# Optimization experiments

Hardware: AMD Instinct MI355X
Metric: run time of the kernel (lower is better)

The kernel has to match this reference:

```python
import jax, jax.numpy as jnp
import numpy as np

D_MODEL = 1024
N_HEADS = 16
HEAD_DIM = D_MODEL // N_HEADS  # 64; note: scores use full d_model dots but sqrt(head_dim) scale
WINDOW = 256
B, S = 4, 4096


def _window_starts(seq_len, ws):
    # replicate the torch loop: half-stride overlapping windows
    stride = ws // 2
    starts = []
    for i in range(0, seq_len, stride):
        end = min(i + ws, seq_len)
        start = max(0, end - ws)
        starts.append(start)
        if end == seq_len:
            break
    return np.asarray(starts, dtype=np.int32)


def setup_inputs() -> dict:
    key = jax.random.key(0)
    ks = jax.random.split(key, 9)
    sc = 0.02
    x = jax.random.normal(ks[0], (B, S, D_MODEL), dtype=jnp.float32)
    Wq = jax.random.normal(ks[1], (D_MODEL, D_MODEL), dtype=jnp.float32) * sc
    bq = jnp.zeros((D_MODEL,), jnp.float32)
    Wk = jax.random.normal(ks[2], (D_MODEL, D_MODEL), dtype=jnp.float32) * sc
    bk = jnp.zeros((D_MODEL,), jnp.float32)
    Wv = jax.random.normal(ks[3], (D_MODEL, D_MODEL), dtype=jnp.float32) * sc
    bv = jnp.zeros((D_MODEL,), jnp.float32)
    Wo = jax.random.normal(ks[4], (D_MODEL, D_MODEL), dtype=jnp.float32) * sc
    bo = jnp.zeros((D_MODEL,), jnp.float32)
    return {"x": x, "Wq": Wq, "bq": bq, "Wk": Wk, "bk": bk,
            "Wv": Wv, "bv": bv, "Wo": Wo, "bo": bo}


def reference(x, Wq, bq, Wk, bk, Wv, bv, Wo, bo):
    Bsz, seq, dm = x.shape
    q = x @ Wq + bq  # [B,S,D] (heads are re-flattened in the windowed path anyway)
    k = x @ Wk + bk
    v = x @ Wv + bv

    starts = _window_starts(seq, WINDOW)            # [W]
    idx = starts[:, None] + np.arange(WINDOW)[None]  # [W, ws] static indices
    idx_j = jnp.asarray(idx)

    qw = q[:, idx_j, :]  # [B, W, ws, D]
    kw = k[:, idx_j, :]
    vw = v[:, idx_j, :]

    scale = 1.0 / np.sqrt(HEAD_DIM).astype(np.float32)
    scores = jnp.einsum('bwid,bwjd->bwij', qw, kw) * scale  # full-d_model dots
    attn = jax.nn.softmax(scores, axis=-1)
    ow = jnp.einsum('bwij,bwjd->bwid', attn, vw)  # [B, W, ws, D]

    flat_idx = idx_j.reshape(-1)  # [W*ws]
    out = jnp.zeros_like(q).at[:, flat_idx, :].add(ow.reshape(Bsz, -1, dm))
    counts = jnp.zeros((seq,), jnp.float32).at[flat_idx].add(1.0)
    out = out / counts[None, :, None]  # overlap-add average

    return out @ Wo + bo
```

## Files before the change

### kernel.cpp

```cpp
#include <hip/hip_runtime.h>
#include <hip/hip_bf16.h>

typedef unsigned short u16;
typedef short bf16x8 __attribute__((ext_vector_type(8)));
typedef float f32x4 __attribute__((ext_vector_type(4)));

#define DM     1024
#define SEQ    4096
#define NBATCH 4
#define NWIN   31
#define NTOK   16384

__device__ __forceinline__ u16 f2b(float f) {
  union { float f; unsigned u; } x; x.f = f;
  unsigned r = (x.u + 0x7fffu + ((x.u >> 16) & 1u)) >> 16;
  return (u16)r;
}
__device__ __forceinline__ float b2f(u16 v) {
  union { unsigned u; float f; } x; x.u = ((unsigned)v) << 16; return x.f;
}
__device__ __forceinline__ void gload_lds16(const u16* g, u16* l) {
  __builtin_amdgcn_global_load_lds(
      (const __attribute__((address_space(1))) void*)g,
      (__attribute__((address_space(3))) void*)l, 16, 0, 0);
}

__global__ __launch_bounds__(256) void k_convert(const float* __restrict__ in,
                                                 u16* __restrict__ out, int n4) {
  int i = blockIdx.x * 256 + threadIdx.x;
  if (i >= n4) return;
  float4 v = ((const float4*)in)[i];
  ushort4 o; o.x = f2b(v.x); o.y = f2b(v.y); o.z = f2b(v.z); o.w = f2b(v.w);
  ((ushort4*)out)[i] = o;
}

__global__ __launch_bounds__(256) void k_transpose4(const float* __restrict__ W0,
                                                    const float* __restrict__ W1,
                                                    const float* __restrict__ W2,
                                                    const float* __restrict__ W3,
                                                    u16* __restrict__ Wt) {
  __shared__ float tile[32][33];
  int z = blockIdx.z;
  const float* W = (z == 0) ? W0 : (z == 1) ? W1 : (z == 2) ? W2 : W3;
  u16* dst = Wt + (size_t)z * DM * DM;
  int n0 = blockIdx.x * 32, k0 = blockIdx.y * 32;
  int tx = threadIdx.x, ty = threadIdx.y;
  #pragma unroll
  for (int i = ty; i < 32; i += 8) tile[i][tx] = W[(size_t)(k0 + i) * DM + n0 + tx];
  __syncthreads();
  #pragma unroll
  for (int i = ty; i < 32; i += 8) dst[(size_t)(n0 + i) * DM + k0 + tx] = f2b(tile[tx][i]);
}

__global__ __launch_bounds__(256) void k_catbias(const float* __restrict__ bq,
                                                 const float* __restrict__ bk,
                                                 const float* __restrict__ bv,
                                                 float* __restrict__ o) {
  int i = blockIdx.x * 256 + threadIdx.x;
  if (i >= 3 * DM) return;
  float v = (i < DM) ? bq[i] : (i < 2 * DM) ? bk[i - DM] : bv[i - 2 * DM];
  o[i] = v;
}

__global__ __launch_bounds__(256, 4) void k_gemm(const u16* __restrict__ A, const u16* __restrict__ Bt,
                                                 const float* __restrict__ bias,
                                                 float* __restrict__ Cf,
                                                 u16* __restrict__ Cb, int ldc,
                                                 u16* __restrict__ Ct, int csplit,
                                                 int M, int N, int K) {
  __shared__ u16 As[128 * 64];
  __shared__ u16 Bs[128 * 64];
  const int tid = threadIdx.x;
  const int wv = tid >> 6, lane = tid & 63;
  const int quad = lane >> 4, l16 = lane & 15;
  const int lr8 = lane >> 3;
  const int lc8 = (((lane & 7) ^ (lr8 & 7)) * 8);
  const int m0 = blockIdx.y * 128, n0 = blockIdx.x * 128;
  const int wm = (wv >> 1) * 64, wn = (wv & 1) * 64;
  const int k7 = l16 & 7;
  f32x4 acc[4][4];
  #pragma unroll
  for (int a = 0; a < 4; ++a)
    #pragma unroll
    for (int b = 0; b < 4; ++b) acc[a][b] = (f32x4){0.f, 0.f, 0.f, 0.f};

  for (int kk = 0; kk < K; kk += 64) {
    #pragma unroll
    for (int j = 0; j < 4; ++j) {
      int e = wv * 4 + j;
      gload_lds16(A + (size_t)(m0 + e * 8 + lr8) * K + kk + lc8, As + e * 512);
    }
    #pragma unroll
    for (int j = 0; j < 4; ++j) {
      int e = wv * 4 + j;
      gload_lds16(Bt + (size_t)(n0 + e * 8 + lr8) * K + kk + lc8, Bs + e * 512);
    }
    __syncthreads();
    #pragma unroll
    for (int h = 0; h < 2; ++h) {
      bf16x8 af[4], bfr[4];
      #pragma unroll
      for (int t = 0; t < 4; ++t)
        af[t]  = *(const bf16x8*)&As[(wm + t * 16 + l16) * 64 + ((h * 4 + quad) ^ k7) * 8];
      #pragma unroll
      for (int t = 0; t < 4; ++t)
        bfr[t] = *(const bf16x8*)&Bs[(wn + t * 16 + l16) * 64 + ((h * 4 + quad) ^ k7) * 8];
      #pragma unroll
      for (int mt = 0; mt < 4; ++mt)
        #pragma unroll
        for (int nt = 0; nt < 4; ++nt)
          acc[mt][nt] = __builtin_amdgcn_mfma_f32_16x16x32_bf16(af[mt], bfr[nt], acc[mt][nt], 0, 0, 0);
    }
    __syncthreads();
  }
  #pragma unroll
  for (int mt = 0; mt < 4; ++mt) {
    #pragma unroll
    for (int nt = 0; nt < 4; ++nt) {
      int row = m0 + wm + mt * 16 + quad * 4;
      int col = n0 + wn + nt * 16 + l16;
      float bv = bias[col];
      if (Cf) {
        #pragma unroll
        for (int r = 0; r < 4; ++r)
          Cf[(size_t)(row + r) * N + col] = acc[mt][nt][r] + bv;
      } else if (col < csplit) {
        #pragma unroll
        for (int r = 0; r < 4; ++r)
          Cb[(size_t)(row + r) * ldc + col] = f2b(acc[mt][nt][r] + bv);
      } else {
        ushort4 o;
        o.x = f2b(acc[mt][nt][0] + bv); o.y = f2b(acc[mt][nt][1] + bv);
        o.z = f2b(acc[mt][nt][2] + bv); o.w = f2b(acc[mt][nt][3] + bv);
        *(ushort4*)&Ct[(size_t)(col - csplit) * M + row] = o;
      }
    }
  }
}

#define LDQ  2048
__global__ __launch_bounds__(256, 2) void k_attn(const u16* __restrict__ QKb, const u16* __restrict__ Vt,
                                                 u16* __restrict__ oA, u16* __restrict__ oB) {
  __shared__ u16 stage[20480];
  __shared__ u16 Pbuf[64 * 256];
  __shared__ float red[2][4][64];
  u16* Qs = stage;
  u16* Ks = stage + 4096;
  u16* Vs = stage;

  const int tid = threadIdx.x;
  const int wv = tid >> 6, lane = tid & 63;
  const int quad = lane >> 4, l16 = lane & 15;
  const int l7 = lane & 7, lr8 = lane >> 3;
  const int kq = (l16 & 7) + (l16 >> 3);

  int id = blockIdx.x;
  int s_ = id >> 3;
  int qt = s_ & 3;
  int pair = (s_ >> 2) * 8 + (id & 7);
  if (pair >= NWIN * NBATCH) return;
  int b = pair / NWIN, w = pair - NWIN * b;

  const int s0 = w * 128;
  const size_t base2 = (size_t)b * SEQ * LDQ;
  const size_t base  = (size_t)b * SEQ * DM;
  const size_t btok  = (size_t)b * SEQ;
  const int qrow0 = s0 + qt * 64;

  f32x4 acc[4][4];
  #pragma unroll
  for (int mt = 0; mt < 4; ++mt)
    #pragma unroll
    for (int nt = 0; nt < 4; ++nt) acc[mt][nt] = (f32x4){0.f, 0.f, 0.f, 0.f};

  for (int kk = 0; kk < DM; kk += 64) {
    #pragma unroll
    for (int j = 0; j < 10; ++j) {
      int idx = wv * 10 + j;
      if (idx < 8) {
        int lc = (l7 ^ ((lr8 + idx) & 7)) * 8;
        gload_lds16(QKb + base2 + (size_t)(qrow0 + idx * 8 + lr8) * LDQ + kk + lc, Qs + idx * 512);
      } else {
        int f = idx - 8;
        int lc = (l7 ^ ((lr8 + f) & 7)) * 8;
        gload_lds16(QKb + DM + base2 + (size_t)(s0 + f * 8 + lr8) * LDQ + kk + lc, Ks + f * 512);
      }
    }
    __syncthreads();
    #pragma unroll
    for (int s2 = 0; s2 < 2; ++s2) {
      bf16x8 aq[4], bk[4];
      #pragma unroll
      for (int mt = 0; mt < 4; ++mt)
        aq[mt] = *(const bf16x8*)&Qs[(mt * 16 + l16) * 64 + (((s2 * 4 + quad) ^ ((kq + 2 * mt) & 7)) * 8)];
      #pragma unroll
      for (int nt = 0; nt < 4; ++nt)
        bk[nt] = *(const bf16x8*)&Ks[(wv * 64 + nt * 16 + l16) * 64 + (((s2 * 4 + quad) ^ ((kq + 2 * nt) & 7)) * 8)];
      #pragma unroll
      for (int mt = 0; mt < 4; ++mt)
        #pragma unroll
        for (int nt = 0; nt < 4; ++nt)
          acc[mt][nt] = __builtin_amdgcn_mfma_f32_16x16x32_bf16(aq[mt], bk[nt], acc[mt][nt], 0, 0, 0);
    }
    __syncthreads();
  }

  float mx[4][4], sm[4][4];
  #pragma unroll
  for (int mt = 0; mt < 4; ++mt)
    #pragma unroll
    for (int r = 0; r < 4; ++r) mx[mt][r] = -1e30f;
  #pragma unroll
  for (int mt = 0; mt < 4; ++mt)
    #pragma unroll
    for (int nt = 0; nt < 4; ++nt)
      #pragma unroll
      for (int r = 0; r < 4; ++r) {
        float v = acc[mt][nt][r] * 0.125f;
        acc[mt][nt][r] = v;
        mx[mt][r] = fmaxf(mx[mt][r], v);
      }
  #pragma unroll
  for (int mt = 0; mt < 4; ++mt)
    #pragma unroll
    for (int r = 0; r < 4; ++r)
      #pragma unroll
      for (int off = 8; off > 0; off >>= 1)
        mx[mt][r] = fmaxf(mx[mt][r], __shfl_xor(mx[mt][r], off, 64));
  if (l16 == 0) {
    #pragma unroll
    for (int mt = 0; mt < 4; ++mt)
      #pragma unroll
      for (int r = 0; r < 4; ++r)
        red[0][wv][mt * 16 + quad * 4 + r] = mx[mt][r];
  }
  __syncthreads();
  float gm[4][4];
  #pragma unroll
  for (int mt = 0; mt < 4; ++mt)
    #pragma unroll
    for (int r = 0; r < 4; ++r) {
      int q = mt * 16 + quad * 4 + r;
      gm[mt][r] = fmaxf(fmaxf(red[0][0][q], red[0][1][q]), fmaxf(red[0][2][q], red[0][3][q]));
      sm[mt][r] = 0.f;
    }
  #pragma unroll
  for (int mt = 0; mt < 4; ++mt)
    #pragma unroll
    for (int nt = 0; nt < 4; ++nt)
      #pragma unroll
      for (int r = 0; r < 4; ++r) {
        float e = __expf(acc[mt][nt][r] - gm[mt][r]);
        acc[mt][nt][r] = e;
        sm[mt][r] += e;
      }
  #pragma unroll
  for (int mt = 0; mt < 4; ++mt)
    #pragma unroll
    for (int r = 0; r < 4; ++r)
      #pragma unroll
      for (int off = 8; off > 0; off >>= 1)
        sm[mt][r] += __shfl_xor(sm[mt][r], off, 64);
  if (l16 == 0) {
    #pragma unroll
    for (int mt = 0; mt < 4; ++mt)
      #pragma unroll
      for (int r = 0; r < 4; ++r)
        red[1][wv][mt * 16 + quad * 4 + r] = sm[mt][r];
  }
  __syncthreads();
  #pragma unroll
  for (int mt = 0; mt < 4; ++mt)
    #pragma unroll
    for (int r = 0; r < 4; ++r) {
      int q = mt * 16 + quad * 4 + r;
      float inv = 1.f / (red[1][0][q] + red[1][1][q] + red[1][2][q] + red[1][3][q]);
      #pragma unroll
      for (int nt = 0; nt < 4; ++nt) {
        int ke = wv * 64 + nt * 16 + l16;
        int phys = (ke >> 3) ^ (q & 7);
        Pbuf[q * 256 + phys * 8 + (ke & 7)] = f2b(acc[mt][nt][r] * inv);
      }
    }
  __syncthreads();

  u16* op = ((w & 1) ? oB : oA) + base;
  for (int slab = 0; slab < 4; ++slab) {
    const int nb = slab * 256;
    f32x4 acc2[4][4];
    #pragma unroll
    for (int mt = 0; mt < 4; ++mt)
      #pragma unroll
      for (int u = 0; u < 4; ++u) acc2[mt][u] = (f32x4){0.f, 0.f, 0.f, 0.f};
    for (int sk = 0; sk < 4; ++sk) {
      const int tok0 = sk * 64;
      #pragma unroll
      for (int j = 0; j < 8; ++j) {
        int e = wv * 8 + j;
        int lc = (l7 ^ ((lr8 + e) & 7)) * 8;
        gload_lds16(Vt + (size_t)(nb + e * 8 + lr8) * NTOK + btok + s0 + tok0 + lc, Vs + e * 512);
      }
      __syncthreads();
      #pragma unroll
      for (int s2 = 0; s2 < 2; ++s2) {
        bf16x8 af[4];
        #pragma unroll
        for (int mt = 0; mt < 4; ++mt) {
          int cP = sk * 8 + s2 * 4 + quad;
          int phys = cP ^ (l16 & 7);
          af[mt] = *(const bf16x8*)&Pbuf[(mt * 16 + l16) * 256 + phys * 8];
        }
        #pragma unroll
        for (int u = 0; u < 4; ++u) {
          bf16x8 bb = *(const bf16x8*)&Vs[(wv * 64 + u * 16 + l16) * 64 +
                                          (((s2 * 4 + quad) ^ ((kq + 2 * u) & 7)) * 8)];
          #pragma unroll
          for (int mt = 0; mt < 4; ++mt)
            acc2[mt][u] = __builtin_amdgcn_mfma_f32_16x16x32_bf16(af[mt], bb, acc2[mt][u], 0, 0, 0);
        }
      }
      __syncthreads();
    }
    #pragma unroll
    for (int mt = 0; mt < 4; ++mt)
      #pragma unroll
      for (int u = 0; u < 4; ++u) {
        int row = qrow0 + mt * 16 + quad * 4;
        int col = nb + wv * 64 + u * 16 + l16;
        #pragma unroll
        for (int r = 0; r < 4; ++r)
          op[(size_t)(row + r) * DM + col] = f2b(acc2[mt][u][r]);
      }
  }
}

__global__ __launch_bounds__(256) void k_norm(const u16* __restrict__ oA, const u16* __restrict__ oB,
                                              u16* __restrict__ out, int n8) {
  int i = blockIdx.x * 256 + threadIdx.x;
  if (i >= n8) return;
  int s = (i >> 7) & (SEQ - 1);
  uint4 a = ((const uint4*)oA)[i];
  uint4 r = a;
  if (s >= 128 && s < 3968) {
    uint4 bq = ((const uint4*)oB)[i];
    const unsigned* ap = (const unsigned*)&a;
    const unsigned* bp = (const unsigned*)&bq;
    unsigned* rp = (unsigned*)&r;
    #pragma unroll
    for (int k = 0; k < 4; ++k) {
      float lo = 0.5f * (b2f((u16)(ap[k] & 0xffff)) + b2f((u16)(bp[k] & 0xffff)));
      float hi = 0.5f * (b2f((u16)(ap[k] >> 16))    + b2f((u16)(bp[k] >> 16)));
      rp[k] = (unsigned)f2b(lo) | ((unsigned)f2b(hi) << 16);
    }
  }
  ((uint4*)out)[i] = r;
}

extern "C" void kernel_launch(void* const* d_in, const int* in_sizes, int n_in,
                              void* d_out, int out_size, void* d_ws, size_t ws_size,
                              hipStream_t stream) {
  const float* x  = (const float*)d_in[0];
  const float* Wq = (const float*)d_in[1];
  const float* bq = (const float*)d_in[2];
  const float* Wk = (const float*)d_in[3];
  const float* bk = (const float*)d_in[4];
  const float* Wv = (const float*)d_in[5];
  const float* bv = (const float*)d_in[6];
  const float* Wo = (const float*)d_in[7];
  const float* bo = (const float*)d_in[8];
  float* out = (float*)d_out;

  char* ws = (char*)d_ws;
  const size_t MB = 1024 * 1024;
  u16*   xb   = (u16*)(ws);
  u16*   qkb  = (u16*)(ws + 32 * MB);
  u16*   vtb  = (u16*)(ws + 96 * MB);
  u16*   wqt  = (u16*)(ws + 128 * MB);
  float* bcat = (float*)(ws + 136 * MB);
  u16*   oA   = (u16*)(ws + 137 * MB);
  u16*   oB   = (u16*)(ws + 169 * MB);

  int n4tok = (int)((size_t)NTOK * DM / 4);
  k_convert<<<(n4tok + 255) / 256, 256, 0, stream>>>(x, xb, n4tok);
  k_transpose4<<<dim3(DM / 32, DM / 32, 4), dim3(32, 8), 0, stream>>>(Wq, Wk, Wv, Wo, wqt);
  k_catbias<<<12, 256, 0, stream>>>(bq, bk, bv, bcat);

  k_gemm<<<dim3(3 * DM / 128, NTOK / 128), 256, 0, stream>>>(
      xb, wqt, bcat, nullptr, qkb, 2048, vtb, 2048, NTOK, 3 * DM, DM);

  k_attn<<<512, 256, 0, stream>>>(qkb, vtb, oA, oB);

  int n8tok = (int)((size_t)NTOK * DM / 8);
  k_norm<<<(n8tok + 255) / 256, 256, 0, stream>>>(oA, oB, xb, n8tok);

  u16* wot = wqt + 3 * (size_t)DM * DM;
  k_gemm<<<dim3(DM / 128, NTOK / 128), 256, 0, stream>>>(
      xb, wot, bo, out, nullptr, DM, nullptr, DM, NTOK, DM, DM);
}
```

Before: 363.4 us.

## Halve attention query tile to 32 rows and fuse prep kernels

The attention kernel now handles 32 query rows per block instead of 64. This doubles the grid to 1024 blocks, shrinks the LDS footprint and register use, and raises the occupancy hint from 2 to 3 blocks. The cost is that the K and V window tiles are loaded twice as often from global memory, so each loaded tile is reused less. Separately, the x conversion, weight transposes and bias concatenation are merged into a single launch to remove launch overhead.

Result: slower. 390.8 us (+7.5%).

```diff
diff --git a/kernel.cpp b/kernel.cpp
--- a/kernel.cpp
+++ b/kernel.cpp
@@ -25,41 +25,42 @@
       (__attribute__((address_space(3))) void*)l, 16, 0, 0);
 }
 
-__global__ __launch_bounds__(256) void k_convert(const float* __restrict__ in,
-                                                 u16* __restrict__ out, int n4) {
-  int i = blockIdx.x * 256 + threadIdx.x;
-  if (i >= n4) return;
-  float4 v = ((const float4*)in)[i];
-  ushort4 o; o.x = f2b(v.x); o.y = f2b(v.y); o.z = f2b(v.z); o.w = f2b(v.w);
-  ((ushort4*)out)[i] = o;
-}
-
-__global__ __launch_bounds__(256) void k_transpose4(const float* __restrict__ W0,
-                                                    const float* __restrict__ W1,
-                                                    const float* __restrict__ W2,
-                                                    const float* __restrict__ W3,
-                                                    u16* __restrict__ Wt) {
+__global__ __launch_bounds__(256) void k_prep(const float* __restrict__ x,
+                                              const float* __restrict__ Wq,
+                                              const float* __restrict__ Wk,
+                                              const float* __restrict__ Wv,
+                                              const float* __restrict__ Wo,
+                                              const float* __restrict__ bq,
+                                              const float* __restrict__ bk,
+                                              const float* __restrict__ bv,
+                                              u16* __restrict__ xb, u16* __restrict__ Wt,
+                                              float* __restrict__ bcat) {
   __shared__ float tile[32][33];
-  int z = blockIdx.z;
-  const float* W = (z == 0) ? W0 : (z == 1) ? W1 : (z == 2) ? W2 : W3;
-  u16* dst = Wt + (size_t)z * DM * DM;
-  int n0 = blockIdx.x * 32, k0 = blockIdx.y * 32;
-  int tx = threadIdx.x, ty = threadIdx.y;
-  #pragma unroll
-  for (int i = ty; i < 32; i += 8) tile[i][tx] = W[(size_t)(k0 + i) * DM + n0 + tx];
-  __syncthreads();
-  #pragma unroll
-  for (int i = ty; i < 32; i += 8) dst[(size_t)(n0 + i) * DM + k0 + tx] = f2b(tile[tx][i]);
-}
-
-__global__ __launch_bounds__(256) void k_catbias(const float* __restrict__ bq,
-                                                 const float* __restrict__ bk,
-                                                 const float* __restrict__ bv,
-                                                 float* __restrict__ o) {
-  int i = blockIdx.x * 256 + threadIdx.x;
-  if (i >= 3 * DM) return;
-  float v = (i < DM) ? bq[i] : (i < 2 * DM) ? bk[i - DM] : bv[i - 2 * DM];
-  o[i] = v;
+  const int id = blockIdx.x, tid = threadIdx.x;
+  if (id < 16384) {
+    int i = id * 256 + tid;
+    float4 v = ((const float4*)x)[i];
+    ushort4 o; o.x = f2b(v.x); o.y = f2b(v.y); o.z = f2b(v.z); o.w = f2b(v.w);
+    ((ushort4*)xb)[i] = o;
+  } else if (id < 20480) {
+    int l = id - 16384;
+    int z = l >> 10, rem = l & 1023;
+    const float* W = (z == 0) ? Wq : (z == 1) ? Wk : (z == 2) ? Wv : Wo;
+    u16* dst = Wt + (size_t)z * DM * DM;
+    int n0 = (rem & 31) * 32, k0 = (rem >> 5) * 32;
+    int tx = tid & 31, ty = tid >> 5;
+    #pragma unroll
+    for (int i = ty; i < 32; i += 8) tile[i][tx] = W[(size_t)(k0 + i) * DM + n0 + tx];
+    __syncthreads();
+    #pragma unroll
+    for (int i = ty; i < 32; i += 8) dst[(size_t)(n0 + i) * DM + k0 + tx] = f2b(tile[tx][i]);
+  } else {
+    int i = (id - 20480) * 256 + tid;
+    if (i < 3 * DM) {
+      float v = (i < DM) ? bq[i] : (i < 2 * DM) ? bk[i - DM] : bv[i - 2 * DM];
+      bcat[i] = v;
+    }
+  }
 }
 
 __global__ __launch_bounds__(256, 4) void k_gemm(const u16* __restrict__ A, const u16* __restrict__ Bt,
@@ -139,13 +140,13 @@
 }
 
 #define LDQ  2048
-__global__ __launch_bounds__(256, 2) void k_attn(const u16* __restrict__ QKb, const u16* __restrict__ Vt,
+__global__ __launch_bounds__(256, 3) void k_attn(const u16* __restrict__ QKb, const u16* __restrict__ Vt,
                                                  u16* __restrict__ oA, u16* __restrict__ oB) {
-  __shared__ u16 stage[20480];
-  __shared__ u16 Pbuf[64 * 256];
-  __shared__ float red[2][4][64];
+  __shared__ u16 stage[18432];
+  __shared__ u16 Pbuf[32 * 256];
+  __shared__ float red[2][4][32];
   u16* Qs = stage;
-  u16* Ks = stage + 4096;
+  u16* Ks = stage + 2048;
   u16* Vs = stage;
 
   const int tid = threadIdx.x;
@@ -156,8 +157,8 @@
 
   int id = blockIdx.x;
   int s_ = id >> 3;
-  int qt = s_ & 3;
-  int pair = (s_ >> 2) * 8 + (id & 7);
+  int qt = s_ & 7;
+  int pair = (s_ >> 3) * 8 + (id & 7);
   if (pair >= NWIN * NBATCH) return;
   int b = pair / NWIN, w = pair - NWIN * b;
 
@@ -165,23 +166,23 @@
   const size_t base2 = (size_t)b * SEQ * LDQ;
   const size_t base  = (size_t)b * SEQ * DM;
   const size_t btok  = (size_t)b * SEQ;
-  const int qrow0 = s0 + qt * 64;
-
-  f32x4 acc[4][4];
-  #pragma unroll
-  for (int mt = 0; mt < 4; ++mt)
+  const int qrow0 = s0 + qt * 32;
+
+  f32x4 acc[2][4];
+  #pragma unroll
+  for (int mt = 0; mt < 2; ++mt)
     #pragma unroll
     for (int nt = 0; nt < 4; ++nt) acc[mt][nt] = (f32x4){0.f, 0.f, 0.f, 0.f};
 
   for (int kk = 0; kk < DM; kk += 64) {
     #pragma unroll
-    for (int j = 0; j < 10; ++j) {
-      int idx = wv * 10 + j;
-      if (idx < 8) {
+    for (int j = 0; j < 9; ++j) {
+      int idx = wv * 9 + j;
+      if (idx < 4) {
         int lc = (l7 ^ ((lr8 + idx) & 7)) * 8;
         gload_lds16(QKb + base2 + (size_t)(qrow0 + idx * 8 + lr8) * LDQ + kk + lc, Qs + idx * 512);
       } else {
-        int f = idx - 8;
+        int f = idx - 4;
         int lc = (l7 ^ ((lr8 + f) & 7)) * 8;
         gload_lds16(QKb + DM + base2 + (size_t)(s0 + f * 8 + lr8) * LDQ + kk + lc, Ks + f * 512);
       }
@@ -189,15 +190,15 @@
     __syncthreads();
     #pragma unroll
     for (int s2 = 0; s2 < 2; ++s2) {
-      bf16x8 aq[4], bk[4];
-      #pragma unroll
-      for (int mt = 0; mt < 4; ++mt)
+      bf16x8 aq[2], bk[4];
+      #pragma unroll
+      for (int mt = 0; mt < 2; ++mt)
         aq[mt] = *(const bf16x8*)&Qs[(mt * 16 + l16) * 64 + (((s2 * 4 + quad) ^ ((kq + 2 * mt) & 7)) * 8)];
       #pragma unroll
       for (int nt = 0; nt < 4; ++nt)
         bk[nt] = *(const bf16x8*)&Ks[(wv * 64 + nt * 16 + l16) * 64 + (((s2 * 4 + quad) ^ ((kq + 2 * nt) & 7)) * 8)];
       #pragma unroll
-      for (int mt = 0; mt < 4; ++mt)
+      for (int mt = 0; mt < 2; ++mt)
         #pragma unroll
         for (int nt = 0; nt < 4; ++nt)
           acc[mt][nt] = __builtin_amdgcn_mfma_f32_16x16x32_bf16(aq[mt], bk[nt], acc[mt][nt], 0, 0, 0);
@@ -205,13 +206,13 @@
     __syncthreads();
   }
 
-  float mx[4][4], sm[4][4];
-  #pragma unroll
-  for (int mt = 0; mt < 4; ++mt)
+  float mx[2][4], sm[2][4];
+  #pragma unroll
+  for (int mt = 0; mt < 2; ++mt)
     #pragma unroll
     for (int r = 0; r < 4; ++r) mx[mt][r] = -1e30f;
   #pragma unroll
-  for (int mt = 0; mt < 4; ++mt)
+  for (int mt = 0; mt < 2; ++mt)
     #pragma unroll
     for (int nt = 0; nt < 4; ++nt)
       #pragma unroll
@@ -221,7 +222,7 @@
         mx[mt][r] = fmaxf(mx[mt][r], v);
       }
   #pragma unroll
-  for (int mt = 0; mt < 4; ++mt)
+  for (int mt = 0; mt < 2; ++mt)
     #pragma unroll
     for (int r = 0; r < 4; ++r)
       #pragma unroll
@@ -229,15 +230,15 @@
         mx[mt][r] = fmaxf(mx[mt][r], __shfl_xor(mx[mt][r], off, 64));
   if (l16 == 0) {
     #pragma unroll
-    for (int mt = 0; mt < 4; ++mt)
+    for (int mt = 0; mt < 2; ++mt)
       #pragma unroll
       for (int r = 0; r < 4; ++r)
         red[0][wv][mt * 16 + quad * 4 + r] = mx[mt][r];
   }
   __syncthreads();
-  float gm[4][4];
-  #pragma unroll
-  for (int mt = 0; mt < 4; ++mt)
+  float gm[2][4];
+  #pragma unroll
+  for (int mt = 0; mt < 2; ++mt)
     #pragma unroll
     for (int r = 0; r < 4; ++r) {
       int q = mt * 16 + quad * 4 + r;
@@ -245,7 +246,7 @@
       sm[mt][r] = 0.f;
     }
   #pragma unroll
-  for (int mt = 0; mt < 4; ++mt)
+  for (int mt = 0; mt < 2; ++mt)
     #pragma unroll
     for (int nt = 0; nt < 4; ++nt)
       #pragma unroll
@@ -255,7 +256,7 @@
         sm[mt][r] += e;
       }
   #pragma unroll
-  for (int mt = 0; mt < 4; ++mt)
+  for (int mt = 0; mt < 2; ++mt)
     #pragma unroll
     for (int r = 0; r < 4; ++r)
       #pragma unroll
@@ -263,14 +264,14 @@
         sm[mt][r] += __shfl_xor(sm[mt][r], off, 64);
   if (l16 == 0) {
     #pragma unroll
-    for (int mt = 0; mt < 4; ++mt)
+    for (int mt = 0; mt < 2; ++mt)
       #pragma unroll
       for (int r = 0; r < 4; ++r)
         red[1][wv][mt * 16 + quad * 4 + r] = sm[mt][r];
   }
   __syncthreads();
   #pragma unroll
-  for (int mt = 0; mt < 4; ++mt)
+  for (int mt = 0; mt < 2; ++mt)
     #pragma unroll
     for (int r = 0; r < 4; ++r) {
       int q = mt * 16 + quad * 4 + r;
@@ -287,9 +288,9 @@
   u16* op = ((w & 1) ? oB : oA) + base;
   for (int slab = 0; slab < 4; ++slab) {
     const int nb = slab * 256;
-    f32x4 acc2[4][4];
-    #pragma unroll
-    for (int mt = 0; mt < 4; ++mt)
+    f32x4 acc2[2][4];
+    #pragma unroll
+    for (int mt = 0; mt < 2; ++mt)
       #pragma unroll
       for (int u = 0; u < 4; ++u) acc2[mt][u] = (f32x4){0.f, 0.f, 0.f, 0.f};
     for (int sk = 0; sk < 4; ++sk) {
@@ -303,9 +304,9 @@
       __syncthreads();
       #pragma unroll
       for (int s2 = 0; s2 < 2; ++s2) {
-        bf16x8 af[4];
-        #pragma unroll
-        for (int mt = 0; mt < 4; ++mt) {
+        bf16x8 af[2];
+        #pragma unroll
+        for (int mt = 0; mt < 2; ++mt) {
           int cP = sk * 8 + s2 * 4 + quad;
           int phys = cP ^ (l16 & 7);
           af[mt] = *(const bf16x8*)&Pbuf[(mt * 16 + l16) * 256 + phys * 8];
@@ -315,14 +316,14 @@
           bf16x8 bb = *(const bf16x8*)&Vs[(wv * 64 + u * 16 + l16) * 64 +
                                           (((s2 * 4 + quad) ^ ((kq + 2 * u) & 7)) * 8)];
           #pragma unroll
-          for (int mt = 0; mt < 4; ++mt)
+          for (int mt = 0; mt < 2; ++mt)
             acc2[mt][u] = __builtin_amdgcn_mfma_f32_16x16x32_bf16(af[mt], bb, acc2[mt][u], 0, 0, 0);
         }
       }
       __syncthreads();
     }
     #pragma unroll
-    for (int mt = 0; mt < 4; ++mt)
+    for (int mt = 0; mt < 2; ++mt)
       #pragma unroll
       for (int u = 0; u < 4; ++u) {
         int row = qrow0 + mt * 16 + quad * 4;
@@ -380,15 +381,12 @@
   u16*   oA   = (u16*)(ws + 137 * MB);
   u16*   oB   = (u16*)(ws + 169 * MB);
 
-  int n4tok = (int)((size_t)NTOK * DM / 4);
-  k_convert<<<(n4tok + 255) / 256, 256, 0, stream>>>(x, xb, n4tok);
-  k_transpose4<<<dim3(DM / 32, DM / 32, 4), dim3(32, 8), 0, stream>>>(Wq, Wk, Wv, Wo, wqt);
-  k_catbias<<<12, 256, 0, stream>>>(bq, bk, bv, bcat);
+  k_prep<<<20492, 256, 0, stream>>>(x, Wq, Wk, Wv, Wo, bq, bk, bv, xb, wqt, bcat);
 
   k_gemm<<<dim3(3 * DM / 128, NTOK / 128), 256, 0, stream>>>(
       xb, wqt, bcat, nullptr, qkb, 2048, vtb, 2048, NTOK, 3 * DM, DM);
 
-  k_attn<<<512, 256, 0, stream>>>(qkb, vtb, oA, oB);
+  k_attn<<<1024, 256, 0, stream>>>(qkb, vtb, oA, oB);
 
   int n8tok = (int)((size_t)NTOK * DM / 8);
   k_norm<<<(n8tok + 255) / 256, 256, 0, stream>>>(oA, oB, xb, n8tok);
```
